# Optimization experiments

Hardware: AMD Instinct MI355X
Metric: run time of the kernel (lower is better)

The kernel has to match this reference:

```python
import jax, jax.numpy as jnp
import numpy as np
from jax import lax

# ---- Haar (db1) wavelet filters, matching create_wavelet_filter ----
_S2 = float(1.0 / np.sqrt(2.0))
_dec_lo = np.array([_S2, _S2], np.float32)    # pywt dec_lo reversed (symmetric)
_dec_hi = np.array([_S2, -_S2], np.float32)   # pywt dec_hi [-s,s] reversed
_rec_lo = np.array([_S2, _S2], np.float32)    # pywt rec_lo flipped (symmetric)
_rec_hi = np.array([-_S2, _S2], np.float32)   # pywt rec_hi [s,-s] flipped

def _outer(a, b):  # torch: a.unsqueeze(0) * b.unsqueeze(1) -> [i,j] = a[j]*b[i]
    return b[:, None] * a[None, :]

DEC = jnp.asarray(np.stack([_outer(_dec_lo, _dec_lo), _outer(_dec_lo, _dec_hi),
                            _outer(_dec_hi, _dec_lo), _outer(_dec_hi, _dec_hi)]))  # [4,2,2]
REC = jnp.asarray(np.stack([_outer(_rec_lo, _rec_lo), _outer(_rec_lo, _rec_hi),
                            _outer(_rec_hi, _rec_lo), _outer(_rec_hi, _rec_hi)]))  # [4,2,2]

BN_EPS = 1e-5

def mish(x):
    return x * jnp.tanh(jax.nn.softplus(x))

def silu(x):
    return x * jax.nn.sigmoid(x)

def bn(x, g, b):  # eval-mode BatchNorm2d with running_mean=0, running_var=1
    return x * (g / jnp.sqrt(1.0 + BN_EPS))[None, :, None, None] + b[None, :, None, None]

def dwconv(x, w, pad):  # depthwise conv, w: [C,1,k,k]
    return lax.conv_general_dilated(x, w, (1, 1), [(pad, pad), (pad, pad)],
                                    feature_group_count=x.shape[1],
                                    dimension_numbers=('NCHW', 'OIHW', 'NCHW'))

def dyn_dwconv(x, ew, gw):
    # DynamicConv2d (depthwise experts). ew: [E,C,1,k,k], gw: [E,C]
    gates = jax.nn.softmax(x.mean((2, 3)) @ gw.T, axis=-1)  # [B,E]
    k = ew.shape[-1]
    outs = jnp.stack([dwconv(x, ew[e], k // 2) for e in range(ew.shape[0])], 1)  # [B,E,C,H,W]
    return jnp.einsum('be,bechw->bchw', gates, outs)

def local_branch(x, ew, gw, bn1g, bn1b, pw, bn2g, bn2b):
    # DWConv2d_BN_ReLU: dynamic dwconv -> BN -> Mish -> depthwise 1x1 (per-channel scale) -> BN
    y = mish(bn(dyn_dwconv(x, ew, gw), bn1g, bn1b))
    y = y * pw[None, :, None, None]
    return bn(y, bn2g, bn2b)

def sel_scan(u, xw, dtw, dtb, Alog, Dp):
    # u: [B,L,D]; xw: [R+2N,D]; dtw: [D,R]; dtb: [D]; Alog: [D,N]; Dp: [D]
    R = dtw.shape[1]
    N = Alog.shape[1]
    xdbl = jnp.einsum('bld,ed->ble', u, xw)
    dt, Bm, Cm = xdbl[..., :R], xdbl[..., R:R + N], xdbl[..., R + N:]
    delta = jax.nn.softplus(jnp.einsum('blr,dr->bld', dt, dtw) + dtb)  # [B,L,D]
    A = -jnp.exp(Alog)                                                  # [D,N]
    a = jnp.exp(delta[..., None] * A)                                   # [B,L,D,N]
    b = delta[..., None] * Bm[:, :, None, :] * u[..., None]             # [B,L,D,N]
    def comb(c1, c2):
        a1, b1 = c1
        a2, b2 = c2
        return a1 * a2, a2 * b1 + b2
    _, h = lax.associative_scan(comb, (a, b), axis=1)                    # h_t = a_t h_{t-1} + b_t
    return jnp.einsum('bldn,bln->bld', h, Cm) + Dp * u

def ss2d(x, in_w, cw, cb, xpw, dtw, dtb, Alog, Dp, ow):
    # SS2D (d_state=1, k_group=2, channel_first): in_proj -> dwconv+silu -> 2-direction
    # selective scan -> gate with silu(z) -> out_proj.
    B, C, H, W = x.shape
    xz = jnp.einsum('oc,bchw->bohw', in_w, x)
    d = in_w.shape[0] // 2
    xi, z = xz[:, :d], xz[:, d:]
    xc = silu(dwconv(xi, cw, 1) + cb[None, :, None, None])
    u0 = xc.reshape(B, d, H * W).transpose(0, 2, 1)                       # row-major scan
    u1 = xc.transpose(0, 1, 3, 2).reshape(B, d, H * W).transpose(0, 2, 1)  # col-major scan
    y0 = sel_scan(u0, xpw[0], dtw[0], dtb[0], Alog[0], Dp[0])
    y1 = sel_scan(u1, xpw[1], dtw[1], dtb[1], Alog[1], Dp[1])
    y0 = y0.transpose(0, 2, 1).reshape(B, d, H, W)
    y1 = y1.transpose(0, 2, 1).reshape(B, d, W, H).transpose(0, 1, 3, 2)
    y = (y0 + y1) * silu(z)
    return jnp.einsum('oc,bchw->bohw', ow, y)

def mbwt(x, wav_w, wav_b, wav_scale, base_scale,
         ss_in_w, ss_conv_w, ss_conv_b, ss_xproj_w, ss_dt_w, ss_dt_b, ss_A_log, ss_D, ss_out_w):
    # MBWTConv2d, wt_levels=1, H/W even. Haar WT (2x2 stride 2) == block reshape + einsum.
    B, C, H, W = x.shape
    xr = x.reshape(B, C, H // 2, 2, W // 2, 2)
    wt = jnp.einsum('bchpwq,kpq->bckhw', xr, DEC)                  # [B,C,4,h,w]
    tag = wt.reshape(B, 4 * C, H // 2, W // 2)
    tag = dwconv(tag, wav_w, wav_w.shape[-1] // 2) + wav_b[None, :, None, None]
    tag = (tag * wav_scale).reshape(B, C, 4, H // 2, W // 2)
    # inverse Haar WT (conv_transpose 2x2 stride 2, groups=C)
    up = jnp.einsum('bckhw,kpq->bchpwq', tag, REC).reshape(B, C, H, W)
    g = ss2d(x, ss_in_w, ss_conv_w, ss_conv_b, ss_xproj_w, ss_dt_w, ss_dt_b, ss_A_log, ss_D, ss_out_w)
    return base_scale * g + up


def setup_inputs() -> dict:
    key = jax.random.key(0)
    ks = iter(jax.random.split(key, 64))
    B, DIM, H, W = 16, 256, 64, 64
    Cg = Cl = 64
    d = {'x': jax.random.normal(next(ks), (B, DIM, H, W), jnp.float32)}
    for j, k in enumerate((3, 5, 7)):
        p = f'l{j}_'
        d[p + 'ew'] = jax.random.normal(next(ks), (4, Cl, 1, k, k), jnp.float32) * 0.1
        d[p + 'gw'] = jax.random.normal(next(ks), (4, Cl), jnp.float32) * 0.1
        d[p + 'bn1g'] = jnp.ones((Cl,), jnp.float32)
        d[p + 'bn1b'] = jnp.zeros((Cl,), jnp.float32)
        d[p + 'pw'] = jax.random.normal(next(ks), (Cl,), jnp.float32) * 0.2
        d[p + 'bn2g'] = jnp.ones((Cl,), jnp.float32)
        d[p + 'bn2b'] = jnp.zeros((Cl,), jnp.float32)
    d['wav_w'] = jax.random.normal(next(ks), (4 * Cg, 1, 3, 3), jnp.float32) * 0.1
    d['wav_b'] = jnp.zeros((4 * Cg,), jnp.float32)
    d['wav_scale'] = jnp.full((1, 4 * Cg, 1, 1), 0.1, jnp.float32)
    d['base_scale'] = jnp.ones((1, Cg, 1, 1), jnp.float32)
    dm, R, N, K = Cg, 4, 1, 2  # d_inner, dt_rank, d_state, k_group
    d['ss_in_w'] = jax.random.normal(next(ks), (2 * dm, Cg), jnp.float32) * float(1 / np.sqrt(Cg))
    d['ss_conv_w'] = jax.random.normal(next(ks), (dm, 1, 3, 3), jnp.float32) * 0.1
    d['ss_conv_b'] = jnp.zeros((dm,), jnp.float32)
    d['ss_xproj_w'] = jax.random.normal(next(ks), (K, R + 2 * N, dm), jnp.float32) * float(1 / np.sqrt(dm))
    d['ss_dt_w'] = jax.random.normal(next(ks), (K, dm, R), jnp.float32) * float(1 / np.sqrt(R))
    d['ss_dt_b'] = jnp.full((K, dm), -2.0, jnp.float32)
    d['ss_A_log'] = jnp.zeros((K, dm, N), jnp.float32)
    d['ss_D'] = jnp.ones((K, dm), jnp.float32)
    d['ss_out_w'] = jax.random.normal(next(ks), (Cg, dm), jnp.float32) * float(1 / np.sqrt(dm))
    return d


def reference(x,
              l0_ew, l0_gw, l0_bn1g, l0_bn1b, l0_pw, l0_bn2g, l0_bn2b,
              l1_ew, l1_gw, l1_bn1g, l1_bn1b, l1_pw, l1_bn2g, l1_bn2b,
              l2_ew, l2_gw, l2_bn1g, l2_bn1b, l2_pw, l2_bn2g, l2_bn2b,
              wav_w, wav_b, wav_scale, base_scale,
              ss_in_w, ss_conv_w, ss_conv_b, ss_xproj_w, ss_dt_w, ss_dt_b, ss_A_log, ss_D, ss_out_w):
    Cg, Cl = 64, 64
    xg, xl, xi = x[:, :Cg], x[:, Cg:Cg + Cl], x[:, Cg + Cl:]
    yl = (local_branch(xl, l0_ew, l0_gw, l0_bn1g, l0_bn1b, l0_pw, l0_bn2g, l0_bn2b)
          + local_branch(xl, l1_ew, l1_gw, l1_bn1g, l1_bn1b, l1_pw, l1_bn2g, l1_bn2b)
          + local_branch(xl, l2_ew, l2_gw, l2_bn1g, l2_bn1b, l2_pw, l2_bn2g, l2_bn2b))
    yg = mbwt(xg, wav_w, wav_b, wav_scale, base_scale,
              ss_in_w, ss_conv_w, ss_conv_b, ss_xproj_w, ss_dt_w, ss_dt_b, ss_A_log, ss_D, ss_out_w)
    return jnp.concatenate([yg, yl, xi], axis=1)
```

## Files before the change

### kernel.cpp

```cpp
#include <hip/hip_runtime.h>
#include <math.h>

static constexpr int NB   = 16;
static constexpr int DIM  = 256;
static constexpr int CG   = 64;
static constexpr int HH   = 64;
static constexpr int WW   = 64;
static constexpr int HW   = HH * WW;

__device__ __forceinline__ float mish_fast(float x) {
    float t = __expf(fminf(x, 20.f));
    float p = __builtin_fmaf(t, t, t + t);
    return x * p * __builtin_amdgcn_rcpf(p + 2.f);
}
__device__ __forceinline__ float silu_f(float x) {
    return x * __builtin_amdgcn_rcpf(1.f + __expf(-x));
}
__device__ __forceinline__ float softplus_fast(float x) {
    return fmaxf(x, 0.f) + __logf(1.f + __expf(-fabsf(x)));
}

__global__ __launch_bounds__(256) void k_stage1(
    const float* __restrict__ x,
    const float* __restrict__ wav_w, const float* __restrict__ wav_b,
    const float* __restrict__ wav_scale,
    float* __restrict__ up, float* __restrict__ mean,
    const float* __restrict__ in_w,
    float* __restrict__ xi, float* __restrict__ z) {
    __shared__ float smem[8192];
    int bid = blockIdx.x;
    int tid = threadIdx.x;

    if (bid % 3 != 2) {
        int aid = (bid / 3) * 2 + (bid % 3);
        int c = aid & 63, b = aid >> 6;
        float* wtb = smem;
        float* red = smem + 4352;
        const float* xp = x + ((size_t)b * DIM + c) * HW;

        {
            const float4* lp4 = (const float4*)(x + ((size_t)b * DIM + 64 + c) * HW);
            float s = 0.f;
            for (int i = tid; i < 1024; i += 256) {
                float4 v = lp4[i];
                s += (v.x + v.y) + (v.z + v.w);
            }
#pragma unroll
            for (int off = 32; off > 0; off >>= 1) s += __shfl_xor(s, off, 64);
            if ((tid & 63) == 0) red[tid >> 6] = s;
            __syncthreads();
            if (tid == 0)
                mean[b * 64 + c] = ((red[0] + red[1]) + (red[2] + red[3])) * (1.f / HW);
        }

#pragma unroll
        for (int it = 0; it < 2; ++it) {
            int p = tid + it * 256;
            int h = p >> 4, w2 = p & 15;
            float4 top = *(const float4*)(xp + (2 * h) * 64 + 4 * w2);
            float4 bot = *(const float4*)(xp + (2 * h + 1) * 64 + 4 * w2);
            float a0 = top.x, b0 = top.y, c0q = bot.x, d0 = bot.y;
            float a1 = top.z, b1 = top.w, c1q = bot.z, d1 = bot.w;
            int base0 = h * 34 + 2 * w2;
            *(float2*)(wtb + 0 * 1088 + base0) =
                make_float2(0.5f * (a0 + b0 + c0q + d0), 0.5f * (a1 + b1 + c1q + d1));
            *(float2*)(wtb + 1 * 1088 + base0) =
                make_float2(0.5f * (a0 + b0 - c0q - d0), 0.5f * (a1 + b1 - c1q - d1));
            *(float2*)(wtb + 2 * 1088 + base0) =
                make_float2(0.5f * (a0 - b0 + c0q - d0), 0.5f * (a1 - b1 + c1q - d1));
            *(float2*)(wtb + 3 * 1088 + base0) =
                make_float2(0.5f * (a0 - b0 - c0q + d0), 0.5f * (a1 - b1 - c1q + d1));
        }
        __syncthreads();

        float wk[4][9], tb[4];
#pragma unroll
        for (int k = 0; k < 4; ++k) {
            int ch = c * 4 + k;
            float sc = wav_scale[ch];
#pragma unroll
            for (int j = 0; j < 9; ++j) wk[k][j] = wav_w[ch * 9 + j] * sc;
            tb[k] = wav_b[ch] * sc;
        }
        float* upp = up + ((size_t)b * CG + c) * HW;
        for (int i = tid; i < 1024; i += 256) {
            int h = i >> 5, w = i & 31;
            float tg[4];
#pragma unroll
            for (int k = 0; k < 4; ++k) {
                float s = tb[k];
#pragma unroll
                for (int dy = -1; dy <= 1; ++dy) {
                    int hh = h + dy;
                    if (hh < 0 || hh >= 32) continue;
#pragma unroll
                    for (int dx = -1; dx <= 1; ++dx) {
                        int wx = w + dx;
                        if (wx < 0 || wx >= 32) continue;
                        s = fmaf(wtb[k * 1088 + hh * 34 + wx], wk[k][(dy + 1) * 3 + (dx + 1)], s);
                    }
                }
                tg[k] = s;
            }
            float u00 = 0.5f * (tg[0] - tg[1] - tg[2] + tg[3]);
            float u01 = 0.5f * (tg[0] - tg[1] + tg[2] - tg[3]);
            float u10 = 0.5f * (tg[0] + tg[1] - tg[2] - tg[3]);
            float u11 = 0.5f * (tg[0] + tg[1] + tg[2] + tg[3]);
            *(float2*)(upp + (2 * h) * 64 + 2 * w)     = make_float2(u00, u01);
            *(float2*)(upp + (2 * h + 1) * 64 + 2 * w) = make_float2(u10, u11);
        }
    } else {
        int id2 = bid / 3;
        int h0 = (id2 & 31) * 2;
        int b  = id2 >> 5;
        float* xs = smem;
        float* wt = smem + 4096;

        float acc[8][8];
#pragma unroll
        for (int i = 0; i < 8; ++i)
#pragma unroll
            for (int j = 0; j < 8; ++j) acc[i][j] = 0.f;

        int o0 = (tid >> 4) * 8;
        int p0 = (tid & 15) * 8;

        for (int ko = 0; ko < 64; ko += 32) {
            if (ko) __syncthreads();
            {
                int s = tid;
#pragma unroll
                for (int it = 0; it < 4; ++it, s += 256) {
                    int c = s >> 5, p4 = (s & 31) * 4;
                    float4 v = *(const float4*)(x + ((size_t)b * DIM + ko + c) * HW + h0 * 64 + p4);
                    *(float4*)(xs + c * 128 + p4) = v;
                }
            }
            {
                int s = tid;
#pragma unroll
                for (int it = 0; it < 4; ++it, s += 256) {
                    int o = s >> 3, c0 = (s & 7) * 4;
#pragma unroll
                    for (int i = 0; i < 4; ++i) {
                        int cc = c0 + i;
                        int osw = o ^ (((cc >> 2) & 3) << 3);
                        wt[cc * 128 + osw] = ((const float*)(in_w + o * 64 + ko + c0))[i];
                    }
                }
            }
            __syncthreads();
#pragma unroll 4
            for (int c = 0; c < 32; ++c) {
                int osw = o0 ^ (((c >> 2) & 3) << 3);
                float xv[8], wv[8];
                *(float4*)(xv)     = *(const float4*)(xs + c * 128 + p0);
                *(float4*)(xv + 4) = *(const float4*)(xs + c * 128 + p0 + 4);
                *(float4*)(wv)     = *(const float4*)(wt + c * 128 + osw);
                *(float4*)(wv + 4) = *(const float4*)(wt + c * 128 + osw + 4);
#pragma unroll
                for (int i = 0; i < 8; ++i)
#pragma unroll
                    for (int j = 0; j < 8; ++j)
                        acc[i][j] = fmaf(wv[i], xv[j], acc[i][j]);
            }
        }

#pragma unroll
        for (int i = 0; i < 8; ++i) {
            int o = o0 + i;
            float* dst = (o < 64) ? (xi + ((size_t)b * 64 + o) * HW + h0 * 64)
                                  : (z + ((size_t)b * 64 + (o - 64)) * HW + h0 * 64);
            *(float4*)(dst + p0)     = make_float4(acc[i][0], acc[i][1], acc[i][2], acc[i][3]);
            *(float4*)(dst + p0 + 4) = make_float4(acc[i][4], acc[i][5], acc[i][6], acc[i][7]);
        }
    }
}

__global__ __launch_bounds__(256) void k_stage2(
    const float* __restrict__ xi,
    const float* __restrict__ cw, const float* __restrict__ cb,
    const float* __restrict__ xpw,
    float* __restrict__ xc, float4* __restrict__ proj4, float2* __restrict__ projBC,
    const float* __restrict__ mean,
    const float* __restrict__ ew3, const float* __restrict__ gw3, const float* __restrict__ g13,
    const float* __restrict__ ew5, const float* __restrict__ gw5, const float* __restrict__ g15,
    const float* __restrict__ ew7, const float* __restrict__ gw7, const float* __restrict__ g17,
    float* __restrict__ w3o, float* __restrict__ w5o, float* __restrict__ w7o) {
    __shared__ float smem[12608];
    int bid = blockIdx.x;
    int tid = threadIdx.x;

    if (bid < 512) {
        int h0 = (bid & 31) * 2;
        int b  = bid >> 5;
        float* xs  = smem;
        float* xcs = smem + 8448;

        int dir = tid >> 7;
        int px  = tid & 127;
        float acc0 = 0.f, acc1 = 0.f, acc2 = 0.f, acc3 = 0.f, acc4 = 0.f, acc5 = 0.f;

        int cl_c = tid >> 3;
        int p0_c = (tid & 7) * 16;
        int row_c = p0_c >> 6;
        int wb_c  = p0_c & 63;

        for (int ch0 = 0; ch0 < 64; ch0 += 32) {
            if (ch0) __syncthreads();
            {
                int s = tid;
#pragma unroll
                for (int it = 0; it < 8; ++it, s += 256) {
                    int c = s >> 6;
                    int rem = s & 63;
                    int r = rem >> 4, w4 = (rem & 15) * 4;
                    int gh = h0 - 1 + r;
                    float4 v = make_float4(0.f, 0.f, 0.f, 0.f);
                    if (gh >= 0 && gh < 64)
                        v = *(const float4*)(xi + ((size_t)b * 64 + ch0 + c) * HW + gh * 64 + w4);
                    float* dp = xs + c * 264 + r * 66 + 1 + w4;
                    dp[0] = v.x; dp[1] = v.y; dp[2] = v.z; dp[3] = v.w;
                }
                if (tid < 128) {
                    int cl = tid >> 2, r = tid & 3;
                    xs[cl * 264 + r * 66 + 0]  = 0.f;
                    xs[cl * 264 + r * 66 + 65] = 0.f;
                }
            }
            __syncthreads();

            {
                float wk[9];
#pragma unroll
                for (int j = 0; j < 9; ++j) wk[j] = cw[(ch0 + cl_c) * 9 + j];
                float bias = cb[ch0 + cl_c];
                float accr[16];
#pragma unroll
                for (int k = 0; k < 16; ++k) accr[k] = bias;
#pragma unroll
                for (int dy = 0; dy < 3; ++dy) {
                    const float* rp = xs + cl_c * 264 + (row_c + dy) * 66 + wb_c;
                    float r[18];
#pragma unroll
                    for (int q = 0; q < 18; ++q) r[q] = rp[q];
#pragma unroll
                    for (int k = 0; k < 16; ++k)
#pragma unroll
                        for (int dx = 0; dx < 3; ++dx)
                            accr[k] = fmaf(r[k + dx], wk[dy * 3 + dx], accr[k]);
                }
#pragma unroll
                for (int k = 0; k < 16; ++k)
                    xcs[cl_c * 130 + p0_c + k] = silu_f(accr[k]);
            }
            __syncthreads();

            {
                int s = tid;
#pragma unroll
                for (int it = 0; it < 4; ++it, s += 256) {
                    int c = s >> 5, pq = (s & 31) * 4;
                    const float* sp = xcs + c * 130 + pq;
                    *(float4*)(xc + ((size_t)b * 64 + ch0 + c) * HW + h0 * 64 + pq) =
                        make_float4(sp[0], sp[1], sp[2], sp[3]);
                }
            }
            {
                const float* wp = xpw + dir * 6 * 64 + ch0;
#pragma unroll 8
                for (int c = 0; c < 32; ++c) {
                    float xv = xcs[c * 130 + px];
                    acc0 = fmaf(xv, wp[0 * 64 + c], acc0);
                    acc1 = fmaf(xv, wp[1 * 64 + c], acc1);
                    acc2 = fmaf(xv, wp[2 * 64 + c], acc2);
                    acc3 = fmaf(xv, wp[3 * 64 + c], acc3);
                    acc4 = fmaf(xv, wp[4 * 64 + c], acc4);
                    acc5 = fmaf(xv, wp[5 * 64 + c], acc5);
                }
            }
        }

        int h = h0 + (px >> 6), w = px & 63;
        int l = (dir == 0) ? (h * 64 + w) : (w * 64 + h);
        size_t base = ((size_t)dir * NB + b) * HW + l;
        proj4[base]  = make_float4(acc0, acc1, acc2, acc3);
        projBC[base] = make_float2(acc4, acc5);
    } else {
        int b = bid - 512;
        int c = tid;
        float* m = smem;
        float* g = smem + 64;
        if (c < 64) m[c] = mean[b * 64 + c];
        __syncthreads();
        const float rs = rsqrtf(1.f + 1e-5f);

#define WEFF_SECT(GW, EW, G1, OUT, K2)                                        \
        {                                                                     \
            if (c < 4) {                                                      \
                float l = 0.f;                                                \
                for (int cc = 0; cc < 64; ++cc) l += m[cc] * GW[c * 64 + cc]; \
                g[c] = l;                                                     \
            }                                                                 \
            __syncthreads();                                                  \
            if (c == 0) {                                                     \
                float mx = fmaxf(fmaxf(g[0], g[1]), fmaxf(g[2], g[3]));       \
                float e0 = expf(g[0] - mx), e1 = expf(g[1] - mx);             \
                float e2 = expf(g[2] - mx), e3 = expf(g[3] - mx);             \
                float inv = 1.f / (e0 + e1 + e2 + e3);                        \
                g[0] = e0 * inv; g[1] = e1 * inv; g[2] = e2 * inv; g[3] = e3 * inv; \
            }                                                                 \
            __syncthreads();                                                  \
            if (c < 64) {                                                     \
                float g1s = G1[c] * rs;                                       \
                for (int kk = 0; kk < K2; ++kk) {                             \
                    float w = 0.f;                                            \
                    for (int e = 0; e < 4; ++e) w += g[e] * EW[(e * 64 + c) * K2 + kk]; \
                    OUT[(b * 64 + c) * K2 + kk] = w * g1s;                    \
                }                                                             \
            }                                                                 \
            __syncthreads();                                                  \
        }

        WEFF_SECT(gw3, ew3, g13, w3o, 9)
        WEFF_SECT(gw5, ew5, g15, w5o, 25)
        WEFF_SECT(gw7, ew7, g17, w7o, 49)
#undef WEFF_SECT
    }
}

__global__ __launch_bounds__(256) void k_scan2(const float* __restrict__ xc,
                                               const float4* __restrict__ proj4,
                                               const float2* __restrict__ projBC,
                                               const float* __restrict__ dt_w,
                                               const float* __restrict__ dt_b,
                                               const float* __restrict__ A_log,
                                               const float* __restrict__ Dp,
                                               const float* __restrict__ z,
                                               float* __restrict__ yz) {
    int wave = threadIdx.x >> 6;
    int lane = threadIdx.x & 63;
    int wid = blockIdx.x;
    int b = wid >> 6;
    int d = wid & 63;

    __shared__ float ut[64 * 65];
    __shared__ float al[4][1088];
    __shared__ float bl[4][1088];
    __shared__ float aggA[4], aggB[4];

    const float* uplane = xc + ((size_t)b * 64 + d) * HW;
    const float4* up4 = (const float4*)uplane;
#pragma unroll
    for (int q = 0; q < 4; ++q) {
        int s = q * 256 + threadIdx.x;
        float4 v = up4[s];
        int r = s >> 4, c0 = (s & 15) * 4;
        float* p = ut + r * 65 + c0;
        p[0] = v.x; p[1] = v.y; p[2] = v.z; p[3] = v.w;
    }
    __syncthreads();

    int ch = wave;
    float* a_my = al[wave];
    float* b_my = bl[wave];
    float y0r[16];

    {
        float4 wv = *(const float4*)(dt_w + d * 4);
        float db = dt_b[d];
        float A = -__expf(A_log[d]);
        float Dv = Dp[d];
        const float4* p4 = proj4 + (size_t)b * HW;
        const float2* pBC = projBC + (size_t)b * HW;

        float uv[16], cm[16];
#pragma unroll
        for (int j = 0; j < 16; ++j) {
            int el = j * 64 + lane;
            int e  = ch * 1024 + el;
            float4 t4 = p4[e];
            float2 t2 = pBC[e];
            float u = ut[(ch * 16 + j) * 65 + lane];
            uv[j] = u; cm[j] = t2.y;
            float pre = fmaf(t4.x, wv.x, fmaf(t4.y, wv.y,
                        fmaf(t4.z, wv.z, fmaf(t4.w, wv.w, db))));
            float delta = softplus_fast(pre);
            float aj = __expf(delta * A);
            float bj = delta * t2.x * u;
            int idx = (el >> 4) * 17 + (el & 15);
            a_my[idx] = aj;
            b_my[idx] = bj;
        }
        __builtin_amdgcn_wave_barrier();

        float a[16], bb[16];
#pragma unroll
        for (int j = 0; j < 16; ++j) {
            a[j]  = a_my[lane * 17 + j];
            bb[j] = b_my[lane * 17 + j];
        }
        float As = 1.f, Bs = 0.f;
#pragma unroll
        for (int j = 0; j < 16; ++j) { Bs = fmaf(a[j], Bs, bb[j]); As *= a[j]; }
        float Ai = As, Bi = Bs;
#pragma unroll
        for (int off = 1; off < 64; off <<= 1) {
            float ap = __shfl_up(Ai, (unsigned)off, 64);
            float bp = __shfl_up(Bi, (unsigned)off, 64);
            if (lane >= off) { Bi = fmaf(Ai, bp, Bi); Ai *= ap; }
        }
        if (lane == 63) { aggA[wave] = Ai; aggB[wave] = Bi; }
        __syncthreads();
        float carry = 0.f;
        for (int k = 0; k < wave; ++k) carry = fmaf(aggA[k], carry, aggB[k]);
        float ap1 = __shfl_up(Ai, 1, 64);
        float bp1 = __shfl_up(Bi, 1, 64);
        float h = (lane == 0) ? carry : fmaf(ap1, carry, bp1);
#pragma unroll
        for (int j = 0; j < 16; ++j) {
            h = fmaf(a[j], h, bb[j]);
            a_my[lane * 17 + j] = h;
        }
        __builtin_amdgcn_wave_barrier();
#pragma unroll
        for (int j = 0; j < 16; ++j) {
            int el = j * 64 + lane;
            float hv = a_my[(el >> 4) * 17 + (el & 15)];
            y0r[j] = fmaf(hv, cm[j], Dv * uv[j]);
        }
    }
    __syncthreads();

    {
        int pd = 64 + d;
        float4 wv = *(const float4*)(dt_w + pd * 4);
        float db = dt_b[pd];
        float A = -__expf(A_log[pd]);
        float Dv = Dp[pd];
        const float4* p4 = proj4 + ((size_t)NB + b) * HW;
        const float2* pBC = projBC + ((size_t)NB + b) * HW;

        float uv[16], cm[16];
#pragma unroll
        for (int j = 0; j < 16; ++j) {
            int el = j * 64 + lane;
            int e  = ch * 1024 + el;
            float4 t4 = p4[e];
            float2 t2 = pBC[e];
            float u = ut[lane * 65 + (ch * 16 + j)];
            uv[j] = u; cm[j] = t2.y;
            float pre = fmaf(t4.x, wv.x, fmaf(t4.y, wv.y,
                        fmaf(t4.z, wv.z, fmaf(t4.w, wv.w, db))));
            float delta = softplus_fast(pre);
            float aj = __expf(delta * A);
            float bj = delta * t2.x * u;
            int idx = (el >> 4) * 17 + (el & 15);
            a_my[idx] = aj;
            b_my[idx] = bj;
        }
        __builtin_amdgcn_wave_barrier();

        float a[16], bb[16];
#pragma unroll
        for (int j = 0; j < 16; ++j) {
            a[j]  = a_my[lane * 17 + j];
            bb[j] = b_my[lane * 17 + j];
        }
        float As = 1.f, Bs = 0.f;
#pragma unroll
        for (int j = 0; j < 16; ++j) { Bs = fmaf(a[j], Bs, bb[j]); As *= a[j]; }
        float Ai = As, Bi = Bs;
#pragma unroll
        for (int off = 1; off < 64; off <<= 1) {
            float ap = __shfl_up(Ai, (unsigned)off, 64);
            float bp = __shfl_up(Bi, (unsigned)off, 64);
            if (lane >= off) { Bi = fmaf(Ai, bp, Bi); Ai *= ap; }
        }
        if (lane == 63) { aggA[wave] = Ai; aggB[wave] = Bi; }
        __syncthreads();
        float carry = 0.f;
        for (int k = 0; k < wave; ++k) carry = fmaf(aggA[k], carry, aggB[k]);
        float ap1 = __shfl_up(Ai, 1, 64);
        float bp1 = __shfl_up(Bi, 1, 64);
        float h = (lane == 0) ? carry : fmaf(ap1, carry, bp1);
#pragma unroll
        for (int j = 0; j < 16; ++j) {
            h = fmaf(a[j], h, bb[j]);
            a_my[lane * 17 + j] = h;
        }
        __builtin_amdgcn_wave_barrier();
#pragma unroll
        for (int j = 0; j < 16; ++j) {
            int el = j * 64 + lane;
            float hv = a_my[(el >> 4) * 17 + (el & 15)];
            ut[lane * 65 + (ch * 16 + j)] = fmaf(hv, cm[j], Dv * uv[j]);
        }
    }
    __syncthreads();

    const float* zp = z + ((size_t)b * 64 + d) * HW;
    float* yp = yz + ((size_t)b * 64 + d) * HW;
#pragma unroll
    for (int j = 0; j < 16; ++j) {
        int e = ch * 1024 + j * 64 + lane;
        float y1v = ut[(ch * 16 + j) * 65 + lane];
        float zz = zp[e];
        yp[e] = (y0r[j] + y1v) * silu_f(zz);
    }
}

__global__ __launch_bounds__(256) void k_stage4(
    const float* __restrict__ x,
    const float* __restrict__ w3, const float* __restrict__ w5, const float* __restrict__ w7,
    const float* __restrict__ b1_0, const float* __restrict__ pw0,
    const float* __restrict__ g2_0, const float* __restrict__ b2_0,
    const float* __restrict__ b1_1, const float* __restrict__ pw1,
    const float* __restrict__ g2_1, const float* __restrict__ b2_1,
    const float* __restrict__ b1_2, const float* __restrict__ pw2,
    const float* __restrict__ g2_2, const float* __restrict__ b2_2,
    const float* __restrict__ yz, const float* __restrict__ ow,
    const float* __restrict__ base_scale, const float* __restrict__ up,
    float* __restrict__ out) {
    __shared__ float smem[6144];
    int bid = blockIdx.x;
    int tid = threadIdx.x;

    if (bid % 9 != 8) {
        int cidx = (bid / 9) * 8 + (bid % 9);
        int tile = cidx & 3;
        int c = (cidx >> 2) & 63;
        int b = cidx >> 8;
        int oy = (tile >> 1) * 32, ox = (tile & 1) * 32;
        float* t = smem;
        const float* xp = x + ((size_t)b * DIM + 64 + c) * HW;
        for (int i = tid; i < 38 * 38; i += 256) {
            int r = i / 38, cc = i % 38;
            int yy = r - 3 + oy, xx = cc - 3 + ox;
            t[r * 40 + cc] = (yy >= 0 && yy < 64 && xx >= 0 && xx < 64) ? xp[yy * 64 + xx] : 0.f;
        }
        {
            const float4* x4 = (const float4*)x;
            float4* o4 = (float4*)out;
            int base = cidx * 512;
#pragma unroll
            for (int it = 0; it < 2; ++it) {
                int idx = base + it * 256 + tid;
                int bb = idx >> 17;
                int r  = idx & 131071;
                int gi = bb * 262144 + 131072 + r;
                o4[gi] = x4[gi];
            }
        }
        const float* w3p = w3 + (b * 64 + c) * 9;
        const float* w5p = w5 + (b * 64 + c) * 25;
        const float* w7p = w7 + (b * 64 + c) * 49;
        float W3r[9], W5r[25], W7r[49];
#pragma unroll
        for (int j = 0; j < 9; ++j)  W3r[j] = w3p[j];
#pragma unroll
        for (int j = 0; j < 25; ++j) W5r[j] = w5p[j];
#pragma unroll
        for (int j = 0; j < 49; ++j) W7r[j] = w7p[j];
        __syncthreads();

        const float rs = rsqrtf(1.f + 1e-5f);
        float bb1a = b1_0[c], bb1b = b1_1[c], bb1c = b1_2[c];
        float ssa = pw0[c] * g2_0[c] * rs, ssb = pw1[c] * g2_1[c] * rs, ssc = pw2[c] * g2_2[c] * rs;
        float bb2a = b2_0[c], bb2b = b2_1[c], bb2c = b2_2[c];

        int y  = tid >> 3;
        int x0 = (tid & 7) * 4;

        float a3[4] = {0.f, 0.f, 0.f, 0.f};
        float a5[4] = {0.f, 0.f, 0.f, 0.f};
        float a7[4] = {0.f, 0.f, 0.f, 0.f};

#pragma unroll
        for (int dy = 0; dy < 7; ++dy) {
            const float4* rp = (const float4*)(t + (y + dy) * 40 + x0);
            float4 q0 = rp[0], q1 = rp[1], q2 = rp[2];
            float r[12] = {q0.x, q0.y, q0.z, q0.w, q1.x, q1.y, q1.z, q1.w,
                           q2.x, q2.y, q2.z, q2.w};
#pragma unroll
            for (int k = 0; k < 4; ++k)
#pragma unroll
                for (int dx = 0; dx < 7; ++dx)
                    a7[k] = fmaf(r[k + dx], W7r[dy * 7 + dx], a7[k]);
            if (dy >= 1 && dy <= 5) {
                int ey = dy - 1;
#pragma unroll
                for (int k = 0; k < 4; ++k)
#pragma unroll
                    for (int dx = 0; dx < 5; ++dx)
                        a5[k] = fmaf(r[k + 1 + dx], W5r[ey * 5 + dx], a5[k]);
            }
            if (dy >= 2 && dy <= 4) {
                int ey = dy - 2;
#pragma unroll
                for (int k = 0; k < 4; ++k)
#pragma unroll
                    for (int dx = 0; dx < 3; ++dx)
                        a3[k] = fmaf(r[k + 2 + dx], W3r[ey * 3 + dx], a3[k]);
            }
        }

        float4 res;
        float* rr = (float*)&res;
#pragma unroll
        for (int k = 0; k < 4; ++k) {
            rr[k] = mish_fast(a3[k] + bb1a) * ssa + bb2a
                  + mish_fast(a5[k] + bb1b) * ssb + bb2b
                  + mish_fast(a7[k] + bb1c) * ssc + bb2c;
        }
        float* op = out + ((size_t)b * DIM + 64 + c) * HW;
        *(float4*)(op + (oy + y) * 64 + ox + x0) = res;
    } else {
        int id2 = bid / 9;
        int h0 = (id2 & 31) * 2;
        int b  = id2 >> 5;
        float* yv = smem;
        float* wt = smem + 4096;

        float acc[8][4];
#pragma unroll
        for (int i = 0; i < 8; ++i)
#pragma unroll
            for (int j = 0; j < 4; ++j) acc[i][j] = 0.f;

        int o0 = (tid >> 5) * 8;
        int p0 = (tid & 31) * 4;

        for (int ko = 0; ko < 64; ko += 32) {
            if (ko) __syncthreads();
            {
                int s = tid;
#pragma unroll
                for (int it = 0; it < 4; ++it, s += 256) {
                    int c = s >> 5, p4 = (s & 31) * 4;
                    size_t idx = ((size_t)b * 64 + ko + c) * HW + h0 * 64 + p4;
                    *(float4*)(yv + c * 128 + p4) = *(const float4*)(yz + idx);
                }
            }
            {
                int s = tid;
#pragma unroll
                for (int it = 0; it < 2; ++it, s += 256) {
                    int o = s >> 3, c0 = (s & 7) * 4;
#pragma unroll
                    for (int i = 0; i < 4; ++i) {
                        int cc = c0 + i;
                        int osw = o ^ (((cc >> 2) & 3) << 3);
                        wt[cc * 64 + osw] = ((const float*)(ow + o * 64 + ko + c0))[i];
                    }
                }
            }
            __syncthreads();
#pragma unroll 4
            for (int c = 0; c < 32; ++c) {
                int osw = o0 ^ (((c >> 2) & 3) << 3);
                float wv[8], xv[4];
                *(float4*)(wv)     = *(const float4*)(wt + c * 64 + osw);
                *(float4*)(wv + 4) = *(const float4*)(wt + c * 64 + osw + 4);
                *(float4*)(xv)     = *(const float4*)(yv + c * 128 + p0);
#pragma unroll
                for (int i = 0; i < 8; ++i)
#pragma unroll
                    for (int j = 0; j < 4; ++j)
                        acc[i][j] = fmaf(wv[i], xv[j], acc[i][j]);
            }
        }

#pragma unroll
        for (int i = 0; i < 8; ++i) {
            int o = o0 + i;
            float bs = base_scale[o];
            float4 u = *(const float4*)(up + ((size_t)b * 64 + o) * HW + h0 * 64 + p0);
            float4 r = make_float4(fmaf(bs, acc[i][0], u.x),
                                   fmaf(bs, acc[i][1], u.y),
                                   fmaf(bs, acc[i][2], u.z),
                                   fmaf(bs, acc[i][3], u.w));
            *(float4*)(out + ((size_t)b * DIM + o) * HW + h0 * 64 + p0) = r;
        }
    }
}

extern "C" void kernel_launch(void* const* d_in, const int* in_sizes, int n_in,
                              void* d_out, int out_size, void* d_ws, size_t ws_size,
                              hipStream_t stream) {
    (void)in_sizes; (void)n_in; (void)out_size; (void)ws_size;
    const float* x = (const float*)d_in[0];
    float* out = (float*)d_out;
    float* ws = (float*)d_ws;

    const size_t IMG = (size_t)NB * 64 * HW;
    float* buf_xi   = ws;
    float* buf_z    = ws + IMG;
    float* buf_xc   = ws + 2 * IMG;
    float* buf_up   = ws + 3 * IMG;
    float* buf_p4   = ws + 4 * IMG;
    float* buf_pBC  = buf_p4 + (size_t)4 * 2 * NB * HW;
    float* buf_mean = buf_pBC + (size_t)2 * 2 * NB * HW;
    float* buf_w3   = buf_mean + 1024;
    float* buf_w5   = buf_w3 + 16 * 64 * 9;
    float* buf_w7   = buf_w5 + 16 * 64 * 25;

    k_stage1<<<1536, 256, 0, stream>>>(x,
        (const float*)d_in[22], (const float*)d_in[23], (const float*)d_in[24],
        buf_up, buf_mean,
        (const float*)d_in[26], buf_xi, buf_z);

    k_stage2<<<528, 256, 0, stream>>>(buf_xi,
        (const float*)d_in[27], (const float*)d_in[28], (const float*)d_in[29],
        buf_xc, (float4*)buf_p4, (float2*)buf_pBC,
        buf_mean,
        (const float*)d_in[1],  (const float*)d_in[2],  (const float*)d_in[3],
        (const float*)d_in[8],  (const float*)d_in[9],  (const float*)d_in[10],
        (const float*)d_in[15], (const float*)d_in[16], (const float*)d_in[17],
        buf_w3, buf_w5, buf_w7);

    k_scan2<<<1024, 256, 0, stream>>>(buf_xc, (const float4*)buf_p4, (const float2*)buf_pBC,
        (const float*)d_in[30], (const float*)d_in[31],
        (const float*)d_in[32], (const float*)d_in[33],
        buf_z, buf_xi);

    k_stage4<<<4608, 256, 0, stream>>>(x, buf_w3, buf_w5, buf_w7,
        (const float*)d_in[4],  (const float*)d_in[5],  (const float*)d_in[6],  (const float*)d_in[7],
        (const float*)d_in[11], (const float*)d_in[12], (const float*)d_in[13], (const float*)d_in[14],
        (const float*)d_in[18], (const float*)d_in[19], (const float*)d_in[20], (const float*)d_in[21],
        buf_xi, (const float*)d_in[34], (const float*)d_in[25], buf_up, out);
}
```

Before: 118.1 us.

## Use half-image tiles with two output rows per thread in local conv

The local-branch depthwise conv blocks now each cover a 32x64 half image instead of a 32x32 quarter, and each thread computes two vertically adjacent output rows from 8 shared-memory row reads instead of 7 per row. The halo is loaded with float4 row copies after a zero fill, instead of scalar bounds-checked loads. The grid shrinks from 4608 to 2560 blocks, with the interleaving ratio changed to 4 conv blocks per GEMM block and the passthrough copy doubled per block. This cuts halo overhead and LDS traffic per output, at the cost of more accumulator registers and an extra barrier.

```diff
diff --git a/kernel.cpp b/kernel.cpp
--- a/kernel.cpp
+++ b/kernel.cpp
@@ -526,25 +526,25 @@
     int bid = blockIdx.x;
     int tid = threadIdx.x;
 
-    if (bid % 9 != 8) {
-        int cidx = (bid / 9) * 8 + (bid % 9);
-        int tile = cidx & 3;
-        int c = (cidx >> 2) & 63;
-        int b = cidx >> 8;
-        int oy = (tile >> 1) * 32, ox = (tile & 1) * 32;
+    if (bid % 5 != 4) {
+        int cidx = (bid / 5) * 4 + (bid % 5);
+        int half = cidx & 1;
+        int c = (cidx >> 1) & 63;
+        int b = cidx >> 7;
+        int oy = half * 32;
         float* t = smem;
         const float* xp = x + ((size_t)b * DIM + 64 + c) * HW;
-        for (int i = tid; i < 38 * 38; i += 256) {
-            int r = i / 38, cc = i % 38;
-            int yy = r - 3 + oy, xx = cc - 3 + ox;
-            t[r * 40 + cc] = (yy >= 0 && yy < 64 && xx >= 0 && xx < 64) ? xp[yy * 64 + xx] : 0.f;
+
+        {
+            float4 z4 = make_float4(0.f, 0.f, 0.f, 0.f);
+            for (int i = tid; i < 684; i += 256) ((float4*)t)[i] = z4;
         }
         {
             const float4* x4 = (const float4*)x;
             float4* o4 = (float4*)out;
-            int base = cidx * 512;
-#pragma unroll
-            for (int it = 0; it < 2; ++it) {
+            int base = cidx * 1024;
+#pragma unroll
+            for (int it = 0; it < 4; ++it) {
                 int idx = base + it * 256 + tid;
                 int bb = idx >> 17;
                 int r  = idx & 131071;
@@ -552,6 +552,15 @@
                 o4[gi] = x4[gi];
             }
         }
+        __syncthreads();
+        {
+            for (int i = tid; i < 608; i += 256) {
+                int tr = i >> 4, q = (i & 15) * 4;
+                int gy = oy + tr - 3;
+                if (gy >= 0 && gy < 64)
+                    *(float4*)(t + tr * 72 + 4 + q) = *(const float4*)(xp + gy * 64 + q);
+            }
+        }
         const float* w3p = w3 + (b * 64 + c) * 9;
         const float* w5p = w5 + (b * 64 + c) * 25;
         const float* w7p = w7 + (b * 64 + c) * 49;
@@ -569,54 +578,78 @@
         float ssa = pw0[c] * g2_0[c] * rs, ssb = pw1[c] * g2_1[c] * rs, ssc = pw2[c] * g2_2[c] * rs;
         float bb2a = b2_0[c], bb2b = b2_1[c], bb2c = b2_2[c];
 
-        int y  = tid >> 3;
-        int x0 = (tid & 7) * 4;
-
-        float a3[4] = {0.f, 0.f, 0.f, 0.f};
-        float a5[4] = {0.f, 0.f, 0.f, 0.f};
-        float a7[4] = {0.f, 0.f, 0.f, 0.f};
-
-#pragma unroll
-        for (int dy = 0; dy < 7; ++dy) {
-            const float4* rp = (const float4*)(t + (y + dy) * 40 + x0);
+        int r  = tid >> 4;
+        int x0 = (tid & 15) * 4;
+
+        float a3[2][4] = {{0.f,0.f,0.f,0.f},{0.f,0.f,0.f,0.f}};
+        float a5[2][4] = {{0.f,0.f,0.f,0.f},{0.f,0.f,0.f,0.f}};
+        float a7[2][4] = {{0.f,0.f,0.f,0.f},{0.f,0.f,0.f,0.f}};
+
+#pragma unroll
+        for (int j = 0; j < 8; ++j) {
+            const float4* rp = (const float4*)(t + (2 * r + j) * 72 + x0);
             float4 q0 = rp[0], q1 = rp[1], q2 = rp[2];
-            float r[12] = {q0.x, q0.y, q0.z, q0.w, q1.x, q1.y, q1.z, q1.w,
-                           q2.x, q2.y, q2.z, q2.w};
-#pragma unroll
-            for (int k = 0; k < 4; ++k)
-#pragma unroll
-                for (int dx = 0; dx < 7; ++dx)
-                    a7[k] = fmaf(r[k + dx], W7r[dy * 7 + dx], a7[k]);
-            if (dy >= 1 && dy <= 5) {
-                int ey = dy - 1;
+            float rr[12] = {q0.x, q0.y, q0.z, q0.w, q1.x, q1.y, q1.z, q1.w,
+                            q2.x, q2.y, q2.z, q2.w};
+            if (j <= 6) {
 #pragma unroll
                 for (int k = 0; k < 4; ++k)
 #pragma unroll
-                    for (int dx = 0; dx < 5; ++dx)
-                        a5[k] = fmaf(r[k + 1 + dx], W5r[ey * 5 + dx], a5[k]);
-            }
-            if (dy >= 2 && dy <= 4) {
-                int ey = dy - 2;
+                    for (int dx = 0; dx < 7; ++dx)
+                        a7[0][k] = fmaf(rr[k + dx + 1], W7r[j * 7 + dx], a7[0][k]);
+                if (j >= 1 && j <= 5) {
+#pragma unroll
+                    for (int k = 0; k < 4; ++k)
+#pragma unroll
+                        for (int dx = 0; dx < 5; ++dx)
+                            a5[0][k] = fmaf(rr[k + dx + 2], W5r[(j - 1) * 5 + dx], a5[0][k]);
+                }
+                if (j >= 2 && j <= 4) {
+#pragma unroll
+                    for (int k = 0; k < 4; ++k)
+#pragma unroll
+                        for (int dx = 0; dx < 3; ++dx)
+                            a3[0][k] = fmaf(rr[k + dx + 3], W3r[(j - 2) * 3 + dx], a3[0][k]);
+                }
+            }
+            if (j >= 1) {
 #pragma unroll
                 for (int k = 0; k < 4; ++k)
 #pragma unroll
-                    for (int dx = 0; dx < 3; ++dx)
-                        a3[k] = fmaf(r[k + 2 + dx], W3r[ey * 3 + dx], a3[k]);
-            }
-        }
-
-        float4 res;
-        float* rr = (float*)&res;
-#pragma unroll
-        for (int k = 0; k < 4; ++k) {
-            rr[k] = mish_fast(a3[k] + bb1a) * ssa + bb2a
-                  + mish_fast(a5[k] + bb1b) * ssb + bb2b
-                  + mish_fast(a7[k] + bb1c) * ssc + bb2c;
-        }
+                    for (int dx = 0; dx < 7; ++dx)
+                        a7[1][k] = fmaf(rr[k + dx + 1], W7r[(j - 1) * 7 + dx], a7[1][k]);
+                if (j >= 2 && j <= 6) {
+#pragma unroll
+                    for (int k = 0; k < 4; ++k)
+#pragma unroll
+                        for (int dx = 0; dx < 5; ++dx)
+                            a5[1][k] = fmaf(rr[k + dx + 2], W5r[(j - 2) * 5 + dx], a5[1][k]);
+                }
+                if (j >= 3 && j <= 5) {
+#pragma unroll
+                    for (int k = 0; k < 4; ++k)
+#pragma unroll
+                        for (int dx = 0; dx < 3; ++dx)
+                            a3[1][k] = fmaf(rr[k + dx + 3], W3r[(j - 3) * 3 + dx], a3[1][k]);
+                }
+            }
+        }
+
         float* op = out + ((size_t)b * DIM + 64 + c) * HW;
-        *(float4*)(op + (oy + y) * 64 + ox + x0) = res;
+#pragma unroll
+        for (int rr2 = 0; rr2 < 2; ++rr2) {
+            float4 res;
+            float* rv = (float*)&res;
+#pragma unroll
+            for (int k = 0; k < 4; ++k) {
+                rv[k] = mish_fast(a3[rr2][k] + bb1a) * ssa + bb2a
+                      + mish_fast(a5[rr2][k] + bb1b) * ssb + bb2b
+                      + mish_fast(a7[rr2][k] + bb1c) * ssc + bb2c;
+            }
+            *(float4*)(op + (oy + 2 * r + rr2) * 64 + x0) = res;
+        }
     } else {
-        int id2 = bid / 9;
+        int id2 = bid / 5;
         int h0 = (id2 & 31) * 2;
         int b  = id2 >> 5;
         float* yv = smem;
@@ -724,7 +757,7 @@
         (const float*)d_in[32], (const float*)d_in[33],
         buf_z, buf_xi);
 
-    k_stage4<<<4608, 256, 0, stream>>>(x, buf_w3, buf_w5, buf_w7,
+    k_stage4<<<2560, 256, 0, stream>>>(x, buf_w3, buf_w5, buf_w7,
         (const float*)d_in[4],  (const float*)d_in[5],  (const float*)d_in[6],  (const float*)d_in[7],
         (const float*)d_in[11], (const float*)d_in[12], (const float*)d_in[13], (const float*)d_in[14],
         (const float*)d_in[18], (const float*)d_in[19], (const float*)d_in[20], (const float*)d_in[21],
```

Result: faster. 114.3 us (-3.2%).
